# Optimization experiments

Measured on AMD Instinct MI355X. Metric: run time of the kernel, lower is better.

## Reference

```python
import jax, jax.numpy as jnp
import numpy as np

N = 80000
E = 1280000
IN_DIM = 512
OUT_DIM = 64
POS_DIM = 8
NEG_SLOPE = 0.01  # F.leaky_relu default


def setup_inputs() -> dict:
    key = jax.random.key(0)
    k1, k2, k3, k4, k5, k6 = jax.random.split(key, 6)
    h = jax.random.normal(k1, (N, IN_DIM), dtype=jnp.float32)
    pos = jax.random.normal(k2, (N, POS_DIM), dtype=jnp.float32)
    src = jax.random.randint(k3, (E,), 0, N, dtype=jnp.int32)
    dst = jax.random.randint(k4, (E,), 0, N, dtype=jnp.int32)
    W_fc = jax.random.normal(k5, (OUT_DIM, IN_DIM), dtype=jnp.float32) * (1.0 / np.sqrt(IN_DIM))
    W_attn = jax.random.normal(k6, (1, 2 * OUT_DIM + 2 * POS_DIM), dtype=jnp.float32) * 0.1
    return {"h": h, "pos": pos, "src": src, "dst": dst, "W_fc": W_fc, "W_attn": W_attn}


def reference(h, pos, src, dst, W_fc, W_attn):
    # node projection: z = fc(h)  [N, out]
    z = h @ W_fc.T
    # attn_fc applied to concat([z_src, z_dst, pos_src, pos_dst]) == split dot products
    wa = W_attn[0]
    w_zs = wa[:OUT_DIM]
    w_zd = wa[OUT_DIM:2 * OUT_DIM]
    w_ps = wa[2 * OUT_DIM:2 * OUT_DIM + POS_DIM]
    w_pd = wa[2 * OUT_DIM + POS_DIM:]
    el = z @ w_zs + pos @ w_ps  # [N] src-side score
    er = z @ w_zd + pos @ w_pd  # [N] dst-side score
    e = el[src] + er[dst]       # [E]
    e = jnp.where(e > 0, e, NEG_SLOPE * e)  # leaky_relu
    # segment softmax over incoming edges of each dst node (numerically stable)
    emax = jax.ops.segment_max(e, dst, num_segments=N)  # [N]
    ex = jnp.exp(e - emax[dst])                         # [E]
    denom = jax.ops.segment_sum(ex, dst, num_segments=N)  # [N]
    alpha = ex / denom[dst]                             # [E]
    # weighted scatter-sum of src features
    msgs = alpha[:, None] * z[src]                      # [E, out]
    h_out = jax.ops.segment_sum(msgs, dst, num_segments=N)  # [N, out]
    return h_out
```

## Files before the change

kernel.cpp:

```cpp
#include <hip/hip_runtime.h>
#include <math.h>

#define N_NODES 80000
#define E_EDGES 1280000
#define IN_DIM  512
#define OUT_DIM 64
#define POS_DIM 8
#define NEG_SLOPE 0.01f

#define NB_BUCKET 1250
#define BCAP 2048
#define SCAT_CHUNK 4096
#define SCAT_NB 313
#define GEMM_NB 625

#define BM 128
#define BK 64
#define LDA 72
#define LDB 72

typedef __attribute__((ext_vector_type(8))) short short8v;
typedef __attribute__((ext_vector_type(4))) float f32x4;

__device__ __forceinline__ unsigned short f2bf(float f) {
    unsigned u = __float_as_uint(f);
    unsigned r = u + 0x7fff + ((u >> 16) & 1);
    return (unsigned short)(r >> 16);
}
__device__ __forceinline__ float lrelu(float e) { return e > 0.f ? e : NEG_SLOPE * e; }

__global__ __launch_bounds__(256) void gemm_scatter(const float* __restrict__ h,
                                                    const float* __restrict__ W,
                                                    const float* __restrict__ pos,
                                                    const float* __restrict__ Wa,
                                                    const int* __restrict__ src,
                                                    const int* __restrict__ dst,
                                                    char* __restrict__ zq,
                                                    float2* __restrict__ el2,
                                                    float* __restrict__ er,
                                                    int* __restrict__ bcnt,
                                                    int* __restrict__ ebuf) {
    __shared__ unsigned short sA[BM][LDA];
    __shared__ unsigned short sB[64][LDB];
    __shared__ int hh[NB_BUCKET];
    __shared__ int gb[NB_BUCKET];
    const int t = threadIdx.x;

    if (blockIdx.x >= GEMM_NB) {
        const int e0 = (blockIdx.x - GEMM_NB) * SCAT_CHUNK;
        for (int i = t; i < NB_BUCKET; i += 256) hh[i] = 0;
        __syncthreads();

        int key[16];
        short bk[16];
        short lr[16];
        #pragma unroll
        for (int r4 = 0; r4 < 4; ++r4) {
            const int e = e0 + r4 * 1024 + (t << 2);
            if (e + 3 < E_EDGES) {
                const int4 s4 = *(const int4*)&src[e];
                const int4 d4 = *(const int4*)&dst[e];
                bk[r4 * 4 + 0] = (short)(d4.x >> 6); key[r4 * 4 + 0] = (s4.x << 6) | (d4.x & 63);
                lr[r4 * 4 + 0] = (short)atomicAdd(&hh[d4.x >> 6], 1);
                bk[r4 * 4 + 1] = (short)(d4.y >> 6); key[r4 * 4 + 1] = (s4.y << 6) | (d4.y & 63);
                lr[r4 * 4 + 1] = (short)atomicAdd(&hh[d4.y >> 6], 1);
                bk[r4 * 4 + 2] = (short)(d4.z >> 6); key[r4 * 4 + 2] = (s4.z << 6) | (d4.z & 63);
                lr[r4 * 4 + 2] = (short)atomicAdd(&hh[d4.z >> 6], 1);
                bk[r4 * 4 + 3] = (short)(d4.w >> 6); key[r4 * 4 + 3] = (s4.w << 6) | (d4.w & 63);
                lr[r4 * 4 + 3] = (short)atomicAdd(&hh[d4.w >> 6], 1);
            } else {
                #pragma unroll
                for (int j = 0; j < 4; ++j) {
                    const int ee = e + j;
                    if (ee < E_EDGES) {
                        const int d = dst[ee];
                        bk[r4 * 4 + j] = (short)(d >> 6);
                        key[r4 * 4 + j] = (src[ee] << 6) | (d & 63);
                        lr[r4 * 4 + j] = (short)atomicAdd(&hh[d >> 6], 1);
                    } else {
                        bk[r4 * 4 + j] = -1;
                    }
                }
            }
        }
        __syncthreads();

        for (int i = t; i < NB_BUCKET; i += 256) {
            const int c = hh[i];
            gb[i] = c ? (i * BCAP + atomicAdd(&bcnt[i], c)) : 0;
        }
        __syncthreads();

        #pragma unroll
        for (int r = 0; r < 16; ++r) {
            if (bk[r] >= 0) {
                ebuf[gb[bk[r]] + lr[r]] = key[r];
            }
        }
        return;
    }

    const int lane = t & 63;
    const int w    = t >> 6;
    const int row0 = blockIdx.x * BM;
    const int g    = lane >> 4;
    const int rr   = lane & 15;

    f32x4 acc[2][4] = {};
    float4 ra[8];
    float4 rb[4];

    {
        #pragma unroll
        for (int i = 0; i < 8; ++i) {
            const int idx = t + i * 256;
            ra[i] = *(const float4*)&h[(size_t)(row0 + (idx >> 4)) * IN_DIM + ((idx & 15) << 2)];
        }
        #pragma unroll
        for (int i = 0; i < 4; ++i) {
            const int idx = t + i * 256;
            rb[i] = *(const float4*)&W[(size_t)(idx >> 4) * IN_DIM + ((idx & 15) << 2)];
        }
    }

    for (int c = 0; c < IN_DIM / BK; ++c) {
        __syncthreads();
        #pragma unroll
        for (int i = 0; i < 8; ++i) {
            const int idx = t + i * 256;
            ushort4 v = {f2bf(ra[i].x), f2bf(ra[i].y), f2bf(ra[i].z), f2bf(ra[i].w)};
            *(ushort4*)&sA[idx >> 4][(idx & 15) << 2] = v;
        }
        #pragma unroll
        for (int i = 0; i < 4; ++i) {
            const int idx = t + i * 256;
            ushort4 v = {f2bf(rb[i].x), f2bf(rb[i].y), f2bf(rb[i].z), f2bf(rb[i].w)};
            *(ushort4*)&sB[idx >> 4][(idx & 15) << 2] = v;
        }
        __syncthreads();

        if (c < IN_DIM / BK - 1) {
            const int k0 = (c + 1) * BK;
            #pragma unroll
            for (int i = 0; i < 8; ++i) {
                const int idx = t + i * 256;
                ra[i] = *(const float4*)&h[(size_t)(row0 + (idx >> 4)) * IN_DIM + k0 + ((idx & 15) << 2)];
            }
            #pragma unroll
            for (int i = 0; i < 4; ++i) {
                const int idx = t + i * 256;
                rb[i] = *(const float4*)&W[(size_t)(idx >> 4) * IN_DIM + k0 + ((idx & 15) << 2)];
            }
        }

        short8v afr[2][2];
        #pragma unroll
        for (int rt = 0; rt < 2; ++rt)
            #pragma unroll
            for (int ks = 0; ks < 2; ++ks)
                afr[rt][ks] = *(const short8v*)&sA[w * 32 + rt * 16 + rr][ks * 32 + g * 8];
        short8v bfr[4][2];
        #pragma unroll
        for (int ct = 0; ct < 4; ++ct)
            #pragma unroll
            for (int ks = 0; ks < 2; ++ks)
                bfr[ct][ks] = *(const short8v*)&sB[ct * 16 + rr][ks * 32 + g * 8];

        #pragma unroll
        for (int ks = 0; ks < 2; ++ks)
            #pragma unroll
            for (int rt = 0; rt < 2; ++rt)
                #pragma unroll
                for (int ct = 0; ct < 4; ++ct)
                    acc[rt][ct] = __builtin_amdgcn_mfma_f32_16x16x32_bf16(
                        afr[rt][ks], bfr[ct][ks], acc[rt][ct], 0, 0, 0);
    }

    __syncthreads();
    char* sI8 = (char*)sB;

    float wzs_c[4], wzd_c[4];
    #pragma unroll
    for (int ct = 0; ct < 4; ++ct) {
        wzs_c[ct] = Wa[ct * 16 + rr];
        wzd_c[ct] = Wa[OUT_DIM + ct * 16 + rr];
    }
    #pragma unroll
    for (int rt = 0; rt < 2; ++rt)
        #pragma unroll
        for (int r = 0; r < 4; ++r) {
            float pe = 0.f, pd = 0.f, rmax = 0.f;
            #pragma unroll
            for (int ct = 0; ct < 4; ++ct) {
                const float v = acc[rt][ct][r];
                pe += v * wzs_c[ct];
                pd += v * wzd_c[ct];
                rmax = fmaxf(rmax, fabsf(v));
            }
            #pragma unroll
            for (int off = 8; off; off >>= 1) {
                pe += __shfl_xor(pe, off);
                pd += __shfl_xor(pd, off);
                rmax = fmaxf(rmax, __shfl_xor(rmax, off));
            }
            rmax = fmaxf(rmax, 1e-20f);
            const float inv_s = 127.f / rmax;
            const int rloc = w * 32 + rt * 16 + g * 4 + r;
            #pragma unroll
            for (int ct = 0; ct < 4; ++ct) {
                int q = __float2int_rn(acc[rt][ct][r] * inv_s);
                q = max(-127, min(127, q));
                sI8[rloc * 64 + ct * 16 + rr] = (char)q;
            }
            if (rr == 0) {
                const int row = row0 + rloc;
                const float4 p0 = *(const float4*)&pos[(size_t)row * POS_DIM];
                const float4 p1 = *(const float4*)&pos[(size_t)row * POS_DIM + 4];
                const float4 s0 = *(const float4*)&Wa[2 * OUT_DIM];
                const float4 s1 = *(const float4*)&Wa[2 * OUT_DIM + 4];
                const float4 d0 = *(const float4*)&Wa[2 * OUT_DIM + POS_DIM];
                const float4 d1 = *(const float4*)&Wa[2 * OUT_DIM + POS_DIM + 4];
                const float elv = pe + p0.x * s0.x + p0.y * s0.y + p0.z * s0.z + p0.w * s0.w
                                     + p1.x * s1.x + p1.y * s1.y + p1.z * s1.z + p1.w * s1.w;
                el2[row] = make_float2(elv, rmax * (1.f / 127.f));
                er[row] = pd + p0.x * d0.x + p0.y * d0.y + p0.z * d0.z + p0.w * d0.w
                              + p1.x * d1.x + p1.y * d1.y + p1.z * d1.z + p1.w * d1.w;
            }
        }

    __syncthreads();
    uint4* g4 = (uint4*)(zq + (size_t)row0 * 64);
    const uint4* s4 = (const uint4*)sI8;
    g4[t] = s4[t];
    g4[t + 256] = s4[t + 256];
}

__global__ __launch_bounds__(256) void csr_aggregate(const int* __restrict__ ebuf,
                                                     const int* __restrict__ bcnt,
                                                     const float2* __restrict__ el2,
                                                     const float* __restrict__ er,
                                                     const char* __restrict__ zq,
                                                     float* __restrict__ out) {
    __shared__ int se[BCAP];
    __shared__ int ss[BCAP];
    __shared__ int cnt[64];
    __shared__ int off0[64];
    __shared__ int cur[64];
    const int b = blockIdx.x;
    const int t = threadIdx.x;
    const int lane = t & 63;
    const int w = t >> 6;
    const int lo = b * BCAP;
    const int ne = min(bcnt[b], BCAP);

    if (t < 64) cnt[t] = 0;
    __syncthreads();

    for (int i4 = t << 2; i4 < ne; i4 += 1024) {
        const int4 k4 = *(const int4*)&ebuf[lo + i4];
        if (i4 + 0 < ne) { se[i4 + 0] = k4.x; atomicAdd(&cnt[k4.x & 63], 1); }
        if (i4 + 1 < ne) { se[i4 + 1] = k4.y; atomicAdd(&cnt[k4.y & 63], 1); }
        if (i4 + 2 < ne) { se[i4 + 2] = k4.z; atomicAdd(&cnt[k4.z & 63], 1); }
        if (i4 + 3 < ne) { se[i4 + 3] = k4.w; atomicAdd(&cnt[k4.w & 63], 1); }
    }
    __syncthreads();

    if (t < 64) {
        const int v = cnt[t];
        int s = v;
        #pragma unroll
        for (int off = 1; off < 64; off <<= 1) {
            const int u = __shfl_up(s, off);
            if (lane >= off) s += u;
        }
        off0[t] = s - v;
        cur[t]  = s - v;
    }
    __syncthreads();

    for (int i4 = t << 2; i4 < ne; i4 += 1024) {
        #pragma unroll
        for (int j = 0; j < 4; ++j) {
            if (i4 + j < ne) {
                const int k = se[i4 + j];
                const int p = atomicAdd(&cur[k & 63], 1);
                ss[p] = k >> 6;
            }
        }
    }
    __syncthreads();

    const int g = lane >> 4;
    const int u = lane & 15;
    const int bl = g << 4;
    for (int r = 0; r < 4; ++r) {
        const int dl = (w << 4) + (r << 2) + g;
        const int d = (b << 6) + dl;
        const int off = off0[dl];
        const int nn = cnt[dl];
        const float erd = er[d];

        int sAi = 0, sBi = 0;
        float eA = -INFINITY, eB = -INFINITY;
        float sclA = 0.f, sclB = 0.f;
        if (u < nn) {
            sAi = ss[off + u];
            const float2 v = el2[sAi];
            sclA = v.y;
            eA = lrelu(v.x + erd);
        }
        if (u + 16 < nn) {
            sBi = ss[off + u + 16];
            const float2 v = el2[sBi];
            sclB = v.y;
            eB = lrelu(v.x + erd);
        }
        float m = fmaxf(eA, eB);
        for (int i = u + 32; i < nn; i += 16)
            m = fmaxf(m, lrelu(el2[ss[off + i]].x + erd));
        #pragma unroll
        for (int off2 = 8; off2; off2 >>= 1) m = fmaxf(m, __shfl_xor(m, off2));

        const float exA = (u < nn) ? __expf(eA - m) : 0.f;
        const float exB = (u + 16 < nn) ? __expf(eB - m) : 0.f;
        float dsum = exA + exB;
        for (int i = u + 32; i < nn; i += 16)
            dsum += __expf(lrelu(el2[ss[off + i]].x + erd) - m);
        #pragma unroll
        for (int off2 = 8; off2; off2 >>= 1) dsum += __shfl_xor(dsum, off2);

        const float exsA = exA * sclA;
        const float exsB = exB * sclB;

        float a0 = 0.f, a1 = 0.f, a2 = 0.f, a3 = 0.f;
        const int nreg = min(nn, 32);
        for (int bb = 0; bb < nreg; bb += 8) {
            float wj[8];
            int sj[8];
            #pragma unroll
            for (int j = 0; j < 8; ++j) {
                const int idx = bb + j;
                wj[j] = (idx < 16) ? __shfl(exsA, bl + idx) : __shfl(exsB, bl + idx - 16);
                sj[j] = (idx < 16) ? __shfl(sAi, bl + idx) : __shfl(sBi, bl + idx - 16);
            }
            #pragma unroll
            for (int j = 0; j < 8; ++j) {
                if (bb + j < nreg) {
                    const char4 z = *(const char4*)&zq[((size_t)sj[j] << 6) + (u << 2)];
                    a0 += wj[j] * (float)z.x; a1 += wj[j] * (float)z.y;
                    a2 += wj[j] * (float)z.z; a3 += wj[j] * (float)z.w;
                }
            }
        }
        for (int i = 32; i < nn; ++i) {
            const int s = ss[off + i];
            const float2 v = el2[s];
            const float wq = __expf(lrelu(v.x + erd) - m) * v.y;
            const char4 z = *(const char4*)&zq[((size_t)s << 6) + (u << 2)];
            a0 += wq * (float)z.x; a1 += wq * (float)z.y;
            a2 += wq * (float)z.z; a3 += wq * (float)z.w;
        }

        const float inv = (nn > 0) ? (1.f / dsum) : 0.f;
        f32x4 o = {a0 * inv, a1 * inv, a2 * inv, a3 * inv};
        __builtin_nontemporal_store(o, (f32x4*)&out[((size_t)d << 6) + (u << 2)]);
    }
}

extern "C" void kernel_launch(void* const* d_in, const int* in_sizes, int n_in,
                              void* d_out, int out_size, void* d_ws, size_t ws_size,
                              hipStream_t stream) {
    const float* h   = (const float*)d_in[0];
    const float* pos = (const float*)d_in[1];
    const int* src   = (const int*)d_in[2];
    const int* dst   = (const int*)d_in[3];
    const float* Wfc = (const float*)d_in[4];
    const float* Wa  = (const float*)d_in[5];
    float* out = (float*)d_out;

    char* ws = (char*)d_ws;
    char*   zq   = (char*)  (ws);
    float2* el2  = (float2*)(ws + 5120000);
    float*  er   = (float*) (ws + 5760000);
    int*    ebuf = (int*)   (ws + 6080000);
    int*    bcnt = (int*)   (ws + 16320000);

    hipMemsetAsync(bcnt, 0, NB_BUCKET * sizeof(int), stream);
    gemm_scatter<<<GEMM_NB + SCAT_NB, 256, 0, stream>>>(h, Wfc, pos, Wa, src, dst,
                                                        zq, el2, er, bcnt, ebuf);
    csr_aggregate<<<NB_BUCKET, 256, 0, stream>>>(ebuf, bcnt, el2, er, zq, out);
}
```

Before: 91.35 us.

## Halve dst bucket size and stage edge scores in shared memory for aggregation

Dst buckets now hold 32 nodes instead of 64, doubling the bucket count and halving per-bucket capacity, so each aggregation block handles fewer nodes and more blocks run at once. The aggregation kernel gathers el2 for all bucket edges into shared memory once. It also stores the exp-weighted scale back into shared memory, so the max, sum and accumulate passes no longer re-gather el2 from global memory. The scatter kernel's shared arrays are unioned into one raw buffer to fit the larger histogram. The risk is overflow: bucket capacity is 1024 for roughly 512 expected edges, with edges past capacity silently dropped as before, and the host launch grid must match the new bucket count.

```diff
diff --git a/kernel.cpp b/kernel.cpp
--- a/kernel.cpp
+++ b/kernel.cpp
@@ -8,8 +8,8 @@
 #define POS_DIM 8
 #define NEG_SLOPE 0.01f
 
-#define NB_BUCKET 1250
-#define BCAP 2048
+#define NB_BUCKET 2500
+#define BCAP 1024
 #define SCAT_CHUNK 4096
 #define SCAT_NB 313
 #define GEMM_NB 625
@@ -40,13 +40,12 @@
                                                     float* __restrict__ er,
                                                     int* __restrict__ bcnt,
                                                     int* __restrict__ ebuf) {
-    __shared__ unsigned short sA[BM][LDA];
-    __shared__ unsigned short sB[64][LDB];
-    __shared__ int hh[NB_BUCKET];
-    __shared__ int gb[NB_BUCKET];
+    __shared__ __align__(16) char smem[27648];
     const int t = threadIdx.x;
 
     if (blockIdx.x >= GEMM_NB) {
+        int* hh = (int*)smem;
+        int* gb = hh + NB_BUCKET;
         const int e0 = (blockIdx.x - GEMM_NB) * SCAT_CHUNK;
         for (int i = t; i < NB_BUCKET; i += 256) hh[i] = 0;
         __syncthreads();
@@ -60,23 +59,23 @@
             if (e + 3 < E_EDGES) {
                 const int4 s4 = *(const int4*)&src[e];
                 const int4 d4 = *(const int4*)&dst[e];
-                bk[r4 * 4 + 0] = (short)(d4.x >> 6); key[r4 * 4 + 0] = (s4.x << 6) | (d4.x & 63);
-                lr[r4 * 4 + 0] = (short)atomicAdd(&hh[d4.x >> 6], 1);
-                bk[r4 * 4 + 1] = (short)(d4.y >> 6); key[r4 * 4 + 1] = (s4.y << 6) | (d4.y & 63);
-                lr[r4 * 4 + 1] = (short)atomicAdd(&hh[d4.y >> 6], 1);
-                bk[r4 * 4 + 2] = (short)(d4.z >> 6); key[r4 * 4 + 2] = (s4.z << 6) | (d4.z & 63);
-                lr[r4 * 4 + 2] = (short)atomicAdd(&hh[d4.z >> 6], 1);
-                bk[r4 * 4 + 3] = (short)(d4.w >> 6); key[r4 * 4 + 3] = (s4.w << 6) | (d4.w & 63);
-                lr[r4 * 4 + 3] = (short)atomicAdd(&hh[d4.w >> 6], 1);
+                bk[r4 * 4 + 0] = (short)(d4.x >> 5); key[r4 * 4 + 0] = (s4.x << 5) | (d4.x & 31);
+                lr[r4 * 4 + 0] = (short)atomicAdd(&hh[d4.x >> 5], 1);
+                bk[r4 * 4 + 1] = (short)(d4.y >> 5); key[r4 * 4 + 1] = (s4.y << 5) | (d4.y & 31);
+                lr[r4 * 4 + 1] = (short)atomicAdd(&hh[d4.y >> 5], 1);
+                bk[r4 * 4 + 2] = (short)(d4.z >> 5); key[r4 * 4 + 2] = (s4.z << 5) | (d4.z & 31);
+                lr[r4 * 4 + 2] = (short)atomicAdd(&hh[d4.z >> 5], 1);
+                bk[r4 * 4 + 3] = (short)(d4.w >> 5); key[r4 * 4 + 3] = (s4.w << 5) | (d4.w & 31);
+                lr[r4 * 4 + 3] = (short)atomicAdd(&hh[d4.w >> 5], 1);
             } else {
                 #pragma unroll
                 for (int j = 0; j < 4; ++j) {
                     const int ee = e + j;
                     if (ee < E_EDGES) {
                         const int d = dst[ee];
-                        bk[r4 * 4 + j] = (short)(d >> 6);
-                        key[r4 * 4 + j] = (src[ee] << 6) | (d & 63);
-                        lr[r4 * 4 + j] = (short)atomicAdd(&hh[d >> 6], 1);
+                        bk[r4 * 4 + j] = (short)(d >> 5);
+                        key[r4 * 4 + j] = (src[ee] << 5) | (d & 31);
+                        lr[r4 * 4 + j] = (short)atomicAdd(&hh[d >> 5], 1);
                     } else {
                         bk[r4 * 4 + j] = -1;
                     }
@@ -100,6 +99,8 @@
         return;
     }
 
+    unsigned short (*sA)[LDA] = (unsigned short(*)[LDA])smem;
+    unsigned short (*sB)[LDB] = (unsigned short(*)[LDB])(smem + BM * LDA * 2);
     const int lane = t & 63;
     const int w    = t >> 6;
     const int row0 = blockIdx.x * BM;
@@ -243,125 +244,114 @@
                                                      float* __restrict__ out) {
     __shared__ int se[BCAP];
     __shared__ int ss[BCAP];
-    __shared__ int cnt[64];
-    __shared__ int off0[64];
-    __shared__ int cur[64];
+    __shared__ float2 sel[BCAP];
+    __shared__ int cnt[32];
+    __shared__ int off0[32];
+    __shared__ int cur[32];
     const int b = blockIdx.x;
     const int t = threadIdx.x;
+    const int lo = b * BCAP;
+    const int ne = min(bcnt[b], BCAP);
+
+    if (t < 32) cnt[t] = 0;
+    __syncthreads();
+
+    {
+        const int i4 = t << 2;
+        if (i4 < ne) {
+            const int4 k4 = *(const int4*)&ebuf[lo + i4];
+            se[i4 + 0] = k4.x; atomicAdd(&cnt[k4.x & 31], 1);
+            if (i4 + 1 < ne) { se[i4 + 1] = k4.y; atomicAdd(&cnt[k4.y & 31], 1); }
+            if (i4 + 2 < ne) { se[i4 + 2] = k4.z; atomicAdd(&cnt[k4.z & 31], 1); }
+            if (i4 + 3 < ne) { se[i4 + 3] = k4.w; atomicAdd(&cnt[k4.w & 31], 1); }
+        }
+    }
+    __syncthreads();
+
+    if (t < 32) {
+        const int v = cnt[t];
+        int s = v;
+        #pragma unroll
+        for (int off = 1; off < 32; off <<= 1) {
+            const int u = __shfl_up(s, off);
+            if (t >= off) s += u;
+        }
+        off0[t] = s - v;
+        cur[t]  = s - v;
+    }
+    __syncthreads();
+
+    {
+        const int i4 = t << 2;
+        if (i4 < ne) {
+            #pragma unroll
+            for (int j = 0; j < 4; ++j) {
+                if (i4 + j < ne) {
+                    const int k = se[i4 + j];
+                    const int p = atomicAdd(&cur[k & 31], 1);
+                    ss[p] = k >> 5;
+                }
+            }
+        }
+    }
+    __syncthreads();
+
+    for (int i = t; i < ne; i += 256) sel[i] = el2[ss[i]];
+    __syncthreads();
+
     const int lane = t & 63;
     const int w = t >> 6;
-    const int lo = b * BCAP;
-    const int ne = min(bcnt[b], BCAP);
-
-    if (t < 64) cnt[t] = 0;
-    __syncthreads();
-
-    for (int i4 = t << 2; i4 < ne; i4 += 1024) {
-        const int4 k4 = *(const int4*)&ebuf[lo + i4];
-        if (i4 + 0 < ne) { se[i4 + 0] = k4.x; atomicAdd(&cnt[k4.x & 63], 1); }
-        if (i4 + 1 < ne) { se[i4 + 1] = k4.y; atomicAdd(&cnt[k4.y & 63], 1); }
-        if (i4 + 2 < ne) { se[i4 + 2] = k4.z; atomicAdd(&cnt[k4.z & 63], 1); }
-        if (i4 + 3 < ne) { se[i4 + 3] = k4.w; atomicAdd(&cnt[k4.w & 63], 1); }
-    }
-    __syncthreads();
-
-    if (t < 64) {
-        const int v = cnt[t];
-        int s = v;
-        #pragma unroll
-        for (int off = 1; off < 64; off <<= 1) {
-            const int u = __shfl_up(s, off);
-            if (lane >= off) s += u;
-        }
-        off0[t] = s - v;
-        cur[t]  = s - v;
-    }
-    __syncthreads();
-
-    for (int i4 = t << 2; i4 < ne; i4 += 1024) {
-        #pragma unroll
-        for (int j = 0; j < 4; ++j) {
-            if (i4 + j < ne) {
-                const int k = se[i4 + j];
-                const int p = atomicAdd(&cur[k & 63], 1);
-                ss[p] = k >> 6;
-            }
-        }
-    }
-    __syncthreads();
-
     const int g = lane >> 4;
     const int u = lane & 15;
-    const int bl = g << 4;
-    for (int r = 0; r < 4; ++r) {
-        const int dl = (w << 4) + (r << 2) + g;
-        const int d = (b << 6) + dl;
+    for (int r = 0; r < 2; ++r) {
+        const int dl = (r << 4) + (w << 2) + g;
+        const int d = (b << 5) + dl;
         const int off = off0[dl];
         const int nn = cnt[dl];
         const float erd = er[d];
 
-        int sAi = 0, sBi = 0;
-        float eA = -INFINITY, eB = -INFINITY;
-        float sclA = 0.f, sclB = 0.f;
-        if (u < nn) {
-            sAi = ss[off + u];
-            const float2 v = el2[sAi];
-            sclA = v.y;
-            eA = lrelu(v.x + erd);
-        }
-        if (u + 16 < nn) {
-            sBi = ss[off + u + 16];
-            const float2 v = el2[sBi];
-            sclB = v.y;
-            eB = lrelu(v.x + erd);
-        }
-        float m = fmaxf(eA, eB);
-        for (int i = u + 32; i < nn; i += 16)
-            m = fmaxf(m, lrelu(el2[ss[off + i]].x + erd));
-        #pragma unroll
-        for (int off2 = 8; off2; off2 >>= 1) m = fmaxf(m, __shfl_xor(m, off2));
-
-        const float exA = (u < nn) ? __expf(eA - m) : 0.f;
-        const float exB = (u + 16 < nn) ? __expf(eB - m) : 0.f;
-        float dsum = exA + exB;
-        for (int i = u + 32; i < nn; i += 16)
-            dsum += __expf(lrelu(el2[ss[off + i]].x + erd) - m);
-        #pragma unroll
-        for (int off2 = 8; off2; off2 >>= 1) dsum += __shfl_xor(dsum, off2);
-
-        const float exsA = exA * sclA;
-        const float exsB = exB * sclB;
+        float m = -INFINITY;
+        for (int i = u; i < nn; i += 16)
+            m = fmaxf(m, lrelu(sel[off + i].x + erd));
+        #pragma unroll
+        for (int o = 8; o; o >>= 1) m = fmaxf(m, __shfl_xor(m, o));
+
+        float ds = 0.f;
+        for (int i = u; i < nn; i += 16) {
+            const float2 v = sel[off + i];
+            const float ex = __expf(lrelu(v.x + erd) - m);
+            ds += ex;
+            sel[off + i].x = ex * v.y;
+        }
+        #pragma unroll
+        for (int o = 8; o; o >>= 1) ds += __shfl_xor(ds, o);
 
         float a0 = 0.f, a1 = 0.f, a2 = 0.f, a3 = 0.f;
-        const int nreg = min(nn, 32);
-        for (int bb = 0; bb < nreg; bb += 8) {
+        int j = 0;
+        for (; j + 8 <= nn; j += 8) {
             float wj[8];
             int sj[8];
             #pragma unroll
-            for (int j = 0; j < 8; ++j) {
-                const int idx = bb + j;
-                wj[j] = (idx < 16) ? __shfl(exsA, bl + idx) : __shfl(exsB, bl + idx - 16);
-                sj[j] = (idx < 16) ? __shfl(sAi, bl + idx) : __shfl(sBi, bl + idx - 16);
-            }
-            #pragma unroll
-            for (int j = 0; j < 8; ++j) {
-                if (bb + j < nreg) {
-                    const char4 z = *(const char4*)&zq[((size_t)sj[j] << 6) + (u << 2)];
-                    a0 += wj[j] * (float)z.x; a1 += wj[j] * (float)z.y;
-                    a2 += wj[j] * (float)z.z; a3 += wj[j] * (float)z.w;
-                }
-            }
-        }
-        for (int i = 32; i < nn; ++i) {
-            const int s = ss[off + i];
-            const float2 v = el2[s];
-            const float wq = __expf(lrelu(v.x + erd) - m) * v.y;
-            const char4 z = *(const char4*)&zq[((size_t)s << 6) + (u << 2)];
-            a0 += wq * (float)z.x; a1 += wq * (float)z.y;
-            a2 += wq * (float)z.z; a3 += wq * (float)z.w;
-        }
-
-        const float inv = (nn > 0) ? (1.f / dsum) : 0.f;
+            for (int k = 0; k < 8; ++k) {
+                wj[k] = sel[off + j + k].x;
+                sj[k] = ss[off + j + k];
+            }
+            #pragma unroll
+            for (int k = 0; k < 8; ++k) {
+                const char4 z = *(const char4*)&zq[((size_t)sj[k] << 6) + (u << 2)];
+                a0 += wj[k] * (float)z.x; a1 += wj[k] * (float)z.y;
+                a2 += wj[k] * (float)z.z; a3 += wj[k] * (float)z.w;
+            }
+        }
+        for (; j < nn; ++j) {
+            const float wv = sel[off + j].x;
+            const int sv = ss[off + j];
+            const char4 z = *(const char4*)&zq[((size_t)sv << 6) + (u << 2)];
+            a0 += wv * (float)z.x; a1 += wv * (float)z.y;
+            a2 += wv * (float)z.z; a3 += wv * (float)z.w;
+        }
+
+        const float inv = (nn > 0) ? (1.f / ds) : 0.f;
         f32x4 o = {a0 * inv, a1 * inv, a2 * inv, a3 * inv};
         __builtin_nontemporal_store(o, (f32x4*)&out[((size_t)d << 6) + (u << 2)]);
     }
```

Result: faster. 85.55 us (-6.4%).
